# Kernel tuning notes

Measured on AMD Instinct MI355X. Metric: run time of the kernel, lower is better.

Reference implementation:

```python
import jax, jax.numpy as jnp
import numpy as np

B_TRIALS = 64   # n_trials
DZ = 512        # latent / network dim
DU = 16         # input dim
DX = 256        # observation dim
T = 1000        # time steps
DECAY = 0.9
G = np.sqrt(2.0)


def setup_inputs() -> dict:
    key = jax.random.key(0)
    k0, k1, k2, k3, k4 = jax.random.split(key, 5)
    z0 = jax.random.normal(k0, (B_TRIALS, DZ), jnp.float32)
    v = jax.random.normal(k1, (B_TRIALS, DU, T), jnp.float32)
    # W ~ (1-decay) * g / sqrt(dz) * N(0,1), per Transition_FullRank init
    W = ((1.0 - DECAY) * G / np.sqrt(DZ)) * jax.random.normal(k2, (DZ, DZ), jnp.float32)
    # Wu: uniform init scaled by 1/sqrt(du)
    Wu = (jax.random.uniform(k3, (DZ, DU), jnp.float32) * 2.0 - 1.0) / np.sqrt(DU)
    h = jnp.zeros((DZ,), jnp.float32)
    # decay_param = log(-log(decay))
    decay_param = jnp.full((1,), np.log(-np.log(DECAY)), jnp.float32)
    # Affine_observation: B ~ sqrt(2/(dz+dv)) * N(0,1), dv=0
    B_obs = np.sqrt(2.0 / DZ) * jax.random.normal(k4, (DZ, DX), jnp.float32)
    Bias = jnp.zeros((DX,), jnp.float32)
    return dict(z0=z0, v=v, W=W, Wu=Wu, h=h, decay_param=decay_param,
                B_obs=B_obs, Bias=Bias)


def reference(z0, v, W, Wu, h, decay_param, B_obs, Bias):
    # decay = exp(-exp(decay_param))
    decay = jnp.exp(-jnp.exp(decay_param[0]))
    v_seq = jnp.transpose(v, (2, 0, 1))  # [T, B, du]

    def step(z, vt):
        # z' = decay*z + W @ relu(z - h) + Wu @ v_t  (per trial)
        z_new = decay * z + jax.nn.relu(z - h) @ W.T + vt @ Wu.T
        return z_new, z_new

    _, zs = jax.lax.scan(step, z0, v_seq)      # [T, B, dz]
    zs = jnp.transpose(zs, (1, 2, 0))          # [B, dz, T]
    # Affine_observation (identity nonlinearity): einsum('zx,bzt->bxt') + bias
    x = jnp.einsum('zx,bzt->bxt', B_obs, zs) + Bias[None, :, None]
    return x
```

## Files before the change

kernel.cpp:

```cpp
#include <hip/hip_runtime.h>

#define DZc 512
#define Bc  64
#define Tc  1000
#define DUc 16
#define DXc 256

#define KTOT 17
#define NFRAG (KTOT * 4)
#define NREG  51
#define NLDS  (NFRAG - NREG)
#define AROW  552


typedef __attribute__((ext_vector_type(4))) float f32x4;
typedef __attribute__((ext_vector_type(8))) short s16x8;

__device__ __forceinline__ unsigned short f2bf(float x) {
  unsigned u = __builtin_bit_cast(unsigned, x);
  u = u + 0x7FFFu + ((u >> 16) & 1u);
  return (unsigned short)(u >> 16);
}
__device__ __forceinline__ float bf2f(unsigned short u) {
  unsigned x = ((unsigned)u) << 16;
  return __builtin_bit_cast(float, x);
}

__global__ void pack_w_kernel(const float* __restrict__ W,
                              const float* __restrict__ Wu,
                              unsigned short* __restrict__ Wp) {
  int d = blockIdx.x * 256 + threadIdx.x;
  int j = d & 7, l = (d >> 3) & 63, nt = (d >> 9) & 31, kt = d >> 14;
  int n = nt * 16 + (l & 15);
  int k = kt * 32 + ((l >> 4) << 3) + j;
  float val = (k < DZc) ? W[n * DZc + k] : Wu[n * DUc + (k & 15)];
  Wp[d] = f2bf(val);
}

__global__ void pack_b_kernel(const float* __restrict__ B,
                              unsigned short* __restrict__ Bp) {
  int d = blockIdx.x * 256 + threadIdx.x;
  int j = d & 7, l = (d >> 3) & 63, nt = (d >> 9) & 15, kt = d >> 13;
  int n = nt * 16 + (l & 15);
  int k = kt * 32 + ((l >> 4) << 3) + j;
  Bp[d] = f2bf(B[k * DXc + n]);
}

__global__ __launch_bounds__(512, 2) void rnn_rec_kernel(
    const float* __restrict__ z0, const float* __restrict__ v,
    const float* __restrict__ h, const float* __restrict__ dp,
    const unsigned short* __restrict__ Wp, unsigned short* __restrict__ zs) {
  __shared__ unsigned short wlds[8][NLDS][512];
  __shared__ unsigned short a_lds[16][AROW];

  const int tid = threadIdx.x;
  const int lane = tid & 63;
  const int w = tid >> 6;
  const int l15 = lane & 15;
  const int lg = lane >> 4;
  const int b0 = blockIdx.x * 16;

  s16x8 wr[NREG];
#pragma unroll
  for (int c = 0; c < NFRAG; ++c) {
    int kt = c >> 2, nt = c & 3;
    s16x8 f = *(const s16x8*)(Wp + ((size_t)((kt * 32 + w * 4 + nt) * 64 + lane)) * 8);
    if (c < NREG) wr[c] = f;
    else *(s16x8*)&wlds[w][c - NREG][lane * 8] = f;
  }

  float hreg[4];
  f32x4 acc[4];
#pragma unroll
  for (int nt = 0; nt < 4; ++nt) {
    hreg[nt] = h[w * 64 + nt * 16 + l15];
#pragma unroll
    for (int r = 0; r < 4; ++r)
      acc[nt][r] = z0[(size_t)(b0 + lg * 4 + r) * DZc + w * 64 + nt * 16 + l15];
  }
  const float decay = expf(-expf(dp[0]));

  const int du = tid & 15, trr = tid >> 4;
  const size_t vbase = ((size_t)(b0 + trr) * DUc + du) * Tc;
  float vcur = (tid < 256) ? v[vbase] : 0.f;

  unsigned short* zbase = zs + (size_t)(b0 + lg * 4) * DZc + w * 64 + l15;

  for (int t = 0; t < Tc; ++t) {
    __syncthreads();
#pragma unroll
    for (int nt = 0; nt < 4; ++nt)
#pragma unroll
      for (int r = 0; r < 4; ++r) {
        float av = acc[nt][r] - hreg[nt];
        av = av > 0.f ? av : 0.f;
        a_lds[lg * 4 + r][w * 64 + nt * 16 + l15] = f2bf(av);
      }
    if (tid < 256) {
      unsigned short hi = f2bf(vcur);
      float rem = vcur - bf2f(hi);
      a_lds[trr][512 + du] = hi;
      a_lds[trr][528 + du] = f2bf(rem);
    }
    float vnext = (tid < 256) ? v[vbase + (t + 1 < Tc ? t + 1 : Tc - 1)] : 0.f;
#pragma unroll
    for (int nt = 0; nt < 4; ++nt)
#pragma unroll
      for (int r = 0; r < 4; ++r) acc[nt][r] *= decay;
    __syncthreads();

#pragma unroll
    for (int kt = 0; kt < KTOT; ++kt) {
      s16x8 af = *(const s16x8*)&a_lds[l15][kt * 32 + lg * 8];
#pragma unroll
      for (int nt = 0; nt < 4; ++nt) {
        int c = kt * 4 + nt;
        s16x8 bf;
        if (c < NREG) bf = wr[c];
        else bf = *(const s16x8*)&wlds[w][c - NREG][lane * 8];
        acc[nt] = __builtin_amdgcn_mfma_f32_16x16x32_bf16(af, bf, acc[nt], 0, 0, 0);
      }
    }

#pragma unroll
    for (int nt = 0; nt < 4; ++nt)
#pragma unroll
      for (int r = 0; r < 4; ++r)
        zbase[r * DZc + nt * 16] = f2bf(acc[nt][r]);
    zbase += Bc * DZc;
    vcur = vnext;
  }
}

__global__ __launch_bounds__(256, 1) void rnn_proj_kernel(
    const unsigned short* __restrict__ zs, const unsigned short* __restrict__ Bp,
    const float* __restrict__ Bias, float* __restrict__ x) {
  const int wg = blockIdx.x;
  const int b = wg / 63;
  const int tbase = (wg % 63) * 16;
  const int tid = threadIdx.x;
  const int lane = tid & 63;
  const int w = tid >> 6;
  const int l15 = lane & 15, lg = lane >> 4;

  const int trow = tbase + l15;
  const int trc = trow < Tc ? trow : Tc - 1;
  const unsigned short* abase = zs + ((size_t)trc * Bc + b) * DZc + lg * 8;
  const s16x8 zz = {0, 0, 0, 0, 0, 0, 0, 0};

  f32x4 acc[4];
#pragma unroll
  for (int n = 0; n < 4; ++n)
#pragma unroll
    for (int e = 0; e < 4; ++e) acc[n][e] = 0.f;

#pragma unroll
  for (int kt = 0; kt < 16; ++kt) {
    s16x8 af = *(const s16x8*)(abase + kt * 32);
    af = (trow < Tc) ? af : zz;
#pragma unroll
    for (int n = 0; n < 4; ++n) {
      s16x8 bf = *(const s16x8*)(Bp + (size_t)((kt * 16 + w * 4 + n) * 64 + lane) * 8);
      acc[n] = __builtin_amdgcn_mfma_f32_16x16x32_bf16(af, bf, acc[n], 0, 0, 0);
    }
  }

  const int t = tbase + lg * 4;
  if (t < Tc) {
#pragma unroll
    for (int n = 0; n < 4; ++n) {
      int xo = (w * 4 + n) * 16 + l15;
      float bias = Bias[xo];
      f32x4 val = acc[n];
#pragma unroll
      for (int e = 0; e < 4; ++e) val[e] += bias;
      *(f32x4*)(x + ((size_t)b * DXc + xo) * Tc + t) = val;
    }
  }
}

extern "C" void kernel_launch(void* const* d_in, const int* in_sizes, int n_in,
                              void* d_out, int out_size, void* d_ws, size_t ws_size,
                              hipStream_t stream) {
  const float* z0   = (const float*)d_in[0];
  const float* v    = (const float*)d_in[1];
  const float* W    = (const float*)d_in[2];
  const float* Wu   = (const float*)d_in[3];
  const float* h    = (const float*)d_in[4];
  const float* dp   = (const float*)d_in[5];
  const float* Bo   = (const float*)d_in[6];
  const float* Bias = (const float*)d_in[7];
  float* x = (float*)d_out;

  unsigned short* Wp = (unsigned short*)d_ws;
  unsigned short* Bp = Wp + 278528;
  unsigned short* zs = Bp + 131072;

  pack_w_kernel<<<1088, 256, 0, stream>>>(W, Wu, Wp);
  pack_b_kernel<<<512, 256, 0, stream>>>(Bo, Bp);
  rnn_rec_kernel<<<4, 512, 0, stream>>>(z0, v, h, dp, Wp, zs);
  rnn_proj_kernel<<<4032, 256, 0, stream>>>(zs, Bp, Bias, x);
}
```

Baseline: 2.075 ms.

## Double-buffer recurrent activations and stream part of W from global each step

```diff
diff --git a/kernel.cpp b/kernel.cpp
--- a/kernel.cpp
+++ b/kernel.cpp
@@ -8,8 +8,9 @@
 
 #define KTOT 17
 #define NFRAG (KTOT * 4)
-#define NREG  51
-#define NLDS  (NFRAG - NREG)
+#define NREG  40
+#define NLDS  12
+#define NSTR  16
 #define AROW  552
 
 
@@ -51,7 +52,7 @@
     const float* __restrict__ h, const float* __restrict__ dp,
     const unsigned short* __restrict__ Wp, unsigned short* __restrict__ zs) {
   __shared__ unsigned short wlds[8][NLDS][512];
-  __shared__ unsigned short a_lds[16][AROW];
+  __shared__ unsigned short abuf[2][16][AROW];
 
   const int tid = threadIdx.x;
   const int lane = tid & 63;
@@ -62,12 +63,13 @@
 
   s16x8 wr[NREG];
 #pragma unroll
-  for (int c = 0; c < NFRAG; ++c) {
+  for (int c = 0; c < NREG + NLDS; ++c) {
     int kt = c >> 2, nt = c & 3;
     s16x8 f = *(const s16x8*)(Wp + ((size_t)((kt * 32 + w * 4 + nt) * 64 + lane)) * 8);
     if (c < NREG) wr[c] = f;
     else *(s16x8*)&wlds[w][c - NREG][lane * 8] = f;
   }
+  const unsigned short* ws_base = Wp + (size_t)(w * 4 * 512 + lane * 8);
 
   float hreg[4];
   f32x4 acc[4];
@@ -84,40 +86,52 @@
   const size_t vbase = ((size_t)(b0 + trr) * DUc + du) * Tc;
   float vcur = (tid < 256) ? v[vbase] : 0.f;
 
+#pragma unroll
+  for (int nt = 0; nt < 4; ++nt)
+#pragma unroll
+    for (int r = 0; r < 4; ++r) {
+      float av = acc[nt][r] - hreg[nt];
+      abuf[0][lg * 4 + r][w * 64 + nt * 16 + l15] = f2bf(av > 0.f ? av : 0.f);
+    }
+  if (tid < 256) {
+    unsigned short hi = f2bf(vcur);
+    abuf[0][trr][512 + du] = hi;
+    abuf[0][trr][528 + du] = f2bf(vcur - bf2f(hi));
+  }
+
   unsigned short* zbase = zs + (size_t)(b0 + lg * 4) * DZc + w * 64 + l15;
 
+  int opaque = 0;
+  int p = 0;
   for (int t = 0; t < Tc; ++t) {
-    __syncthreads();
+    asm volatile("" : "+v"(opaque));
+    const unsigned short* wsp = ws_base + opaque;
+
+    asm volatile("s_waitcnt lgkmcnt(0)\n\ts_barrier" ::: "memory");
+
+    float vnext = (tid < 256) ? v[vbase + (t + 1 < Tc ? t + 1 : Tc - 1)] : 0.f;
+
 #pragma unroll
     for (int nt = 0; nt < 4; ++nt)
 #pragma unroll
-      for (int r = 0; r < 4; ++r) {
-        float av = acc[nt][r] - hreg[nt];
-        av = av > 0.f ? av : 0.f;
-        a_lds[lg * 4 + r][w * 64 + nt * 16 + l15] = f2bf(av);
-      }
-    if (tid < 256) {
-      unsigned short hi = f2bf(vcur);
-      float rem = vcur - bf2f(hi);
-      a_lds[trr][512 + du] = hi;
-      a_lds[trr][528 + du] = f2bf(rem);
-    }
-    float vnext = (tid < 256) ? v[vbase + (t + 1 < Tc ? t + 1 : Tc - 1)] : 0.f;
-#pragma unroll
-    for (int nt = 0; nt < 4; ++nt)
-#pragma unroll
       for (int r = 0; r < 4; ++r) acc[nt][r] *= decay;
-    __syncthreads();
-
+
+    s16x8 sbuf[NSTR];
 #pragma unroll
     for (int kt = 0; kt < KTOT; ++kt) {
-      s16x8 af = *(const s16x8*)&a_lds[l15][kt * 32 + lg * 8];
+#pragma unroll
+      for (int c = NREG + NLDS; c < NFRAG; ++c)
+        if ((c >> 2) == kt + 2)
+          sbuf[c - NREG - NLDS] =
+              *(const s16x8*)(wsp + (size_t)(c >> 2) * 16384 + (c & 3) * 512);
+
+      s16x8 af = *(const s16x8*)&abuf[p][l15][kt * 32 + lg * 8];
 #pragma unroll
       for (int nt = 0; nt < 4; ++nt) {
         int c = kt * 4 + nt;
-        s16x8 bf;
-        if (c < NREG) bf = wr[c];
-        else bf = *(const s16x8*)&wlds[w][c - NREG][lane * 8];
+        s16x8 bf = (c < NREG) ? wr[c]
+                 : (c < NREG + NLDS) ? *(const s16x8*)&wlds[w][c - NREG][lane * 8]
+                 : sbuf[c - NREG - NLDS];
         acc[nt] = __builtin_amdgcn_mfma_f32_16x16x32_bf16(af, bf, acc[nt], 0, 0, 0);
       }
     }
@@ -128,6 +142,20 @@
       for (int r = 0; r < 4; ++r)
         zbase[r * DZc + nt * 16] = f2bf(acc[nt][r]);
     zbase += Bc * DZc;
+
+#pragma unroll
+    for (int nt = 0; nt < 4; ++nt)
+#pragma unroll
+      for (int r = 0; r < 4; ++r) {
+        float av = acc[nt][r] - hreg[nt];
+        abuf[p ^ 1][lg * 4 + r][w * 64 + nt * 16 + l15] = f2bf(av > 0.f ? av : 0.f);
+      }
+    if (tid < 256) {
+      unsigned short hi = f2bf(vnext);
+      abuf[p ^ 1][trr][512 + du] = hi;
+      abuf[p ^ 1][trr][528 + du] = f2bf(vnext - bf2f(hi));
+    }
+    p ^= 1;
     vcur = vnext;
   }
 }
```

Result: slower. 2.280 ms (+9.9%).
